# Optimization experiments

Hardware: AMD Instinct MI355X
Metric: run time of the kernel (lower is better)

## Reference

```python
import jax, jax.numpy as jnp
import numpy as np

B, N, CIN = 8, 16384, 256
G, K, C, H, L = 16, 128, 256, 8, 2


def setup_inputs() -> dict:
    key = jax.random.key(0)
    ks = jax.random.split(key, 8)
    f = lambda k, s: jax.random.normal(k, s, dtype=jnp.float32)
    return dict(
        x=f(ks[0], (B, N, CIN)),
        W_lin=f(ks[1], (CIN, C)) * 0.02,
        b_lin=jnp.zeros((C,), jnp.float32),
        emb=f(ks[2], (G, K, C)),  # learned_embedding ~ randn in torch
        in_proj_w=f(ks[3], (L, 3 * C, C)) * 0.02,
        in_proj_b=jnp.zeros((L, 3 * C), jnp.float32),
        out_w=f(ks[4], (L, C, C)) * 0.02,
        out_b=jnp.zeros((L, C), jnp.float32),
        lin_w=f(ks[5], (L, C, C)) * 0.02,
        lin_b=jnp.zeros((L, C), jnp.float32),
        ln1_w=jnp.ones((L, C), jnp.float32),
        ln1_b=jnp.zeros((L, C), jnp.float32),
        ln2_w=jnp.ones((L, C), jnp.float32),
        ln2_b=jnp.zeros((L, C), jnp.float32),
    )


def _layernorm(x, w, b, eps=1e-5):
    m = x.mean(-1, keepdims=True)
    v = jnp.var(x, axis=-1, keepdims=True)
    return (x - m) / jnp.sqrt(v + eps) * w + b


def reference(x, W_lin, b_lin, emb, in_proj_w, in_proj_b, out_w, out_b,
              lin_w, lin_b, ln1_w, ln1_b, ln2_w, ln2_b):
    B_, N_, Cin = x.shape
    T = N_ // G  # tokens per group
    # grouped projection: [B,G,T,C]
    x4 = x.reshape(B_, G, T, Cin) @ W_lin + b_lin
    # cross-attn scores [B,G,K,T]; softmax over the LATENT axis k (dim=-2)
    scores = jnp.einsum('gkd,bgtd->bgkt', emb, x4) * (1.0 / jnp.sqrt(jnp.float32(C)))
    attn = jax.nn.softmax(scores, axis=2)
    y = jnp.einsum('bgkt,bgtd->bgkd', attn, x4)  # [B,G,K,C]
    # torch MHA with batch_first=False: (B*G) is SEQUENCE, K is BATCH
    y = y.reshape(B_ * G, K, C)  # (S, Nb, C)
    S = B_ * G
    Dh = C // H
    scale = 1.0 / jnp.sqrt(jnp.float32(Dh))
    for i in range(L):
        qkv = y @ in_proj_w[i].T + in_proj_b[i]
        q, k, v = jnp.split(qkv, 3, axis=-1)
        q = q.reshape(S, K, H, Dh)
        k = k.reshape(S, K, H, Dh)
        v = v.reshape(S, K, H, Dh)
        s2 = jnp.einsum('snhd,tnhd->nhst', q, k) * scale  # (Nb,H,S,S)
        a = jax.nn.softmax(s2, axis=-1)
        o = jnp.einsum('nhst,tnhd->snhd', a, v).reshape(S, K, C)
        o = o @ out_w[i].T + out_b[i]
        y = _layernorm(o + y, ln1_w[i], ln1_b[i])
        y = _layernorm(y @ lin_w[i].T + lin_b[i] + y, ln2_w[i], ln2_b[i])
    out = y.reshape(B_, G * K, C)
    return (out, attn)
```

## Files before the change

kernel.cpp:

```cpp
#include <hip/hip_runtime.h>

typedef __attribute__((ext_vector_type(4))) float  f32x4;
typedef __attribute__((ext_vector_type(8))) short  s16x8;
typedef __attribute__((ext_vector_type(4))) short  s16x4;

static __device__ __forceinline__ short f2bf(float f) {
    unsigned int x = __builtin_bit_cast(unsigned int, f);
    x += 0x7fffu + ((x >> 16) & 1u);
    return (short)(x >> 16);
}

__global__ __launch_bounds__(256) void castall(
    const float* __restrict__ emb, const float* __restrict__ ipw,
    const float* __restrict__ outw, const float* __restrict__ linw,
    short* __restrict__ de, short* __restrict__ di,
    short* __restrict__ dg, short* __restrict__ dl)
{
    int q = blockIdx.x * 256 + threadIdx.x;
    const float* s; short* d; int o;
    if (q < 131072)      { s = emb;  d = de; o = q; }
    else if (q < 229376) { s = ipw;  d = di; o = q - 131072; }
    else if (q < 262144) { s = outw; d = dg; o = q - 229376; }
    else                 { s = linw; d = dl; o = q - 262144; }
    f32x4 v = *(const f32x4*)(s + (size_t)o * 4);
    s16x4 r;
    #pragma unroll
    for (int j = 0; j < 4; ++j) r[j] = f2bf(v[j]);
    *(s16x4*)(d + (size_t)o * 4) = r;
}

__global__ __launch_bounds__(256) void tcast256(const float* __restrict__ in,
                                                short* __restrict__ out) {
    out[blockIdx.x * 256 + threadIdx.x] = f2bf(in[threadIdx.x * 256 + blockIdx.x]);
}

template<bool AF32, bool OF32, bool OB16>
__global__ __launch_bounds__(256) void gemm_rb(
    const void* __restrict__ Av, const short* __restrict__ Bm,
    const float* __restrict__ bias,
    float* __restrict__ Cf, short* __restrict__ Cb,
    int M, int N)
{
    __shared__ short lsB[128 * 256];
    const int tid = threadIdx.x;
    const int m0 = blockIdx.x * 128;
    const int n0 = blockIdx.y * 128;
    const int lane = tid & 63;
    const int w = tid >> 6;
    const int wmi = w >> 1, wni = w & 1;
    const int lr = lane & 15, ko = lane >> 4;

    {
        const int r0 = tid >> 1, hb = tid & 1;
        const short* Bp = Bm + (size_t)(n0 + r0) * 256 + hb * 128;
        const int sw = (r0 & 7) << 4;
        char* dst = (char*)(lsB + r0 * 256);
        #pragma unroll
        for (int i = 0; i < 16; ++i) {
            int cb = (hb * 16 + i) * 16;
            *(s16x8*)(dst + (cb ^ sw)) = *(const s16x8*)(Bp + i * 8);
        }
    }
    __syncthreads();

    const int swr = (lr & 7) << 4;
    f32x4 acc[4][4] = {};
    #pragma unroll
    for (int ks = 0; ks < 8; ++ks) {
        const int k0 = ks * 32;
        s16x8 af[4];
        #pragma unroll
        for (int mt = 0; mt < 4; ++mt) {
            const int rowA = m0 + wmi * 64 + mt * 16 + lr;
            if constexpr (AF32) {
                const float* Ap = (const float*)Av + (size_t)rowA * 256 + k0 + ko * 8;
                f32x4 x0 = *(const f32x4*)Ap;
                f32x4 x1 = *(const f32x4*)(Ap + 4);
                #pragma unroll
                for (int j = 0; j < 4; ++j) { af[mt][j] = f2bf(x0[j]); af[mt][4 + j] = f2bf(x1[j]); }
            } else {
                const short* Ap = (const short*)Av + (size_t)rowA * 256 + k0 + ko * 8;
                af[mt] = *(const s16x8*)Ap;
            }
        }
        s16x8 bf[4];
        #pragma unroll
        for (int nt = 0; nt < 4; ++nt) {
            const int nrow = wni * 64 + nt * 16 + lr;
            bf[nt] = *(const s16x8*)((const char*)(lsB + nrow * 256) + ((k0 * 2 + ko * 16) ^ swr));
        }
        #pragma unroll
        for (int mt = 0; mt < 4; ++mt)
            #pragma unroll
            for (int nt = 0; nt < 4; ++nt)
                acc[mt][nt] = __builtin_amdgcn_mfma_f32_16x16x32_bf16(af[mt], bf[nt], acc[mt][nt], 0, 0, 0);
    }
    const int cr = ko * 4, cc = lr;
    #pragma unroll
    for (int mt = 0; mt < 4; ++mt)
    #pragma unroll
    for (int nt = 0; nt < 4; ++nt) {
        const int col = n0 + wni * 64 + nt * 16 + cc;
        const float bv = bias ? bias[col] : 0.f;
        #pragma unroll
        for (int j = 0; j < 4; ++j) {
            const int row = m0 + wmi * 64 + mt * 16 + cr + j;
            float v = acc[mt][nt][j] + bv;
            size_t idx = (size_t)row * N + col;
            if constexpr (OF32) Cf[idx] = v;
            if constexpr (OB16) Cb[idx] = f2bf(v);
        }
    }
}

__global__ __launch_bounds__(256) void scores_softmax(
    const short* __restrict__ embb, const short* __restrict__ x4b,
    float* __restrict__ attnF, short* __restrict__ attnB)
{
    __shared__ short lsA[128 * 256];
    float* redm = (float*)lsA;
    float* reds = redm + 256;
    const int tid = threadIdx.x;
    const int z = blockIdx.y;
    const int g = z & 15;
    const int t0 = blockIdx.x * 128;
    const short* A = embb + (size_t)g * 32768;
    const short* B = x4b + (size_t)z * 262144 + (size_t)t0 * 256;
    const int lane = tid & 63;
    const int w = tid >> 6;
    const int wmi = w >> 1, wni = w & 1;
    const int lr = lane & 15, ko = lane >> 4;

    {
        const int r0 = tid >> 1, hb = tid & 1;
        const short* Ap = A + (size_t)r0 * 256 + hb * 128;
        const int sw = (r0 & 7) << 4;
        char* dst = (char*)(lsA + r0 * 256);
        #pragma unroll
        for (int i = 0; i < 16; ++i) {
            int cb = (hb * 16 + i) * 16;
            *(s16x8*)(dst + (cb ^ sw)) = *(const s16x8*)(Ap + i * 8);
        }
    }
    __syncthreads();

    const int swr = (lr & 7) << 4;
    f32x4 acc[4][4] = {};
    #pragma unroll
    for (int ks = 0; ks < 8; ++ks) {
        const int k0 = ks * 32;
        s16x8 af[4];
        #pragma unroll
        for (int mt = 0; mt < 4; ++mt) {
            const int krow = wmi * 64 + mt * 16 + lr;
            af[mt] = *(const s16x8*)((const char*)(lsA + krow * 256) + ((k0 * 2 + ko * 16) ^ swr));
        }
        s16x8 bf[4];
        #pragma unroll
        for (int nt = 0; nt < 4; ++nt) {
            const int trow = wni * 64 + nt * 16 + lr;
            bf[nt] = *(const s16x8*)(B + (size_t)trow * 256 + k0 + ko * 8);
        }
        #pragma unroll
        for (int mt = 0; mt < 4; ++mt)
            #pragma unroll
            for (int nt = 0; nt < 4; ++nt)
                acc[mt][nt] = __builtin_amdgcn_mfma_f32_16x16x32_bf16(af[mt], bf[nt], acc[mt][nt], 0, 0, 0);
    }
    __syncthreads();

    const float scale = 0.0625f;
    float cm[4];
    #pragma unroll
    for (int nt = 0; nt < 4; ++nt) {
        float m = -1e30f;
        #pragma unroll
        for (int mt = 0; mt < 4; ++mt)
            #pragma unroll
            for (int j = 0; j < 4; ++j) m = fmaxf(m, acc[mt][nt][j]);
        m = fmaxf(m, __shfl_xor(m, 16));
        m = fmaxf(m, __shfl_xor(m, 32));
        cm[nt] = m * scale;
    }
    if (lane < 16) {
        #pragma unroll
        for (int nt = 0; nt < 4; ++nt)
            redm[wmi * 128 + wni * 64 + nt * 16 + lr] = cm[nt];
    }
    __syncthreads();
    float cmax[4];
    #pragma unroll
    for (int nt = 0; nt < 4; ++nt) {
        int c = wni * 64 + nt * 16 + lr;
        cmax[nt] = fmaxf(redm[c], redm[128 + c]);
    }
    float cs[4];
    #pragma unroll
    for (int nt = 0; nt < 4; ++nt) {
        float s = 0.f;
        #pragma unroll
        for (int mt = 0; mt < 4; ++mt)
            #pragma unroll
            for (int j = 0; j < 4; ++j) {
                float p = __expf(acc[mt][nt][j] * scale - cmax[nt]);
                acc[mt][nt][j] = p;
                s += p;
            }
        s += __shfl_xor(s, 16);
        s += __shfl_xor(s, 32);
        cs[nt] = s;
    }
    if (lane < 16) {
        #pragma unroll
        for (int nt = 0; nt < 4; ++nt)
            reds[wmi * 128 + wni * 64 + nt * 16 + lr] = cs[nt];
    }
    __syncthreads();
    #pragma unroll
    for (int nt = 0; nt < 4; ++nt) {
        int c = wni * 64 + nt * 16 + lr;
        float inv = 1.f / (reds[c] + reds[128 + c]);
        int col = t0 + c;
        #pragma unroll
        for (int mt = 0; mt < 4; ++mt)
            #pragma unroll
            for (int j = 0; j < 4; ++j) {
                int row = wmi * 64 + mt * 16 + ko * 4 + j;
                float a = acc[mt][nt][j] * inv;
                size_t idx = ((size_t)(z * 128 + row)) * 1024 + col;
                attnF[idx] = a;
                attnB[idx] = f2bf(a);
            }
    }
}

__global__ __launch_bounds__(256) void y_gemm(
    const short* __restrict__ attnB, const short* __restrict__ x4b,
    float* __restrict__ yF, short* __restrict__ yB)
{
    __shared__ short lsA[128 * 40];
    __shared__ short lsB[128 * 40];
    const int tid = threadIdx.x;
    const int z = blockIdx.y;
    const int d0 = blockIdx.x * 128;
    const short* A = attnB + (size_t)z * 131072;
    const short* X = x4b + (size_t)z * 262144 + d0;
    const int lane = tid & 63;
    const int w = tid >> 6;
    const int wmi = w >> 1, wni = w & 1;
    const int lr = lane & 15, ko = lane >> 4;
    const int r0 = tid >> 1, oc0 = (tid * 2) & 3;
    const int rb = tid >> 3, ocb = (tid * 2) & 15;

    const short* Ap = A + (size_t)r0 * 1024 + oc0 * 8;
    const short* Xp = X + (size_t)rb * 256 + ocb * 8;

    s16x8 pa0 = *(const s16x8*)(Ap);
    s16x8 pa1 = *(const s16x8*)(Ap + 8);
    s16x8 pv0 = *(const s16x8*)(Xp);
    s16x8 pv1 = *(const s16x8*)(Xp + 8);

    f32x4 acc[4][4] = {};
    for (int k0 = 0; k0 < 1024; k0 += 32) {
        *(s16x8*)&lsA[r0 * 40 + oc0 * 8]     = pa0;
        *(s16x8*)&lsA[r0 * 40 + oc0 * 8 + 8] = pa1;
        #pragma unroll
        for (int j = 0; j < 8; ++j) {
            int dd = ocb * 8 + j;
            lsB[dd * 40 + ((((rb >> 3) ^ ((dd >> 4) & 3)) << 3) | (rb & 7))] = pv0[j];
            int dd2 = dd + 8;
            lsB[dd2 * 40 + ((((rb >> 3) ^ ((dd2 >> 4) & 3)) << 3) | (rb & 7))] = pv1[j];
        }
        __syncthreads();
        if (k0 + 32 < 1024) {
            pa0 = *(const s16x8*)(Ap + k0 + 32);
            pa1 = *(const s16x8*)(Ap + k0 + 40);
            pv0 = *(const s16x8*)(Xp + (size_t)(k0 + 32) * 256);
            pv1 = *(const s16x8*)(Xp + (size_t)(k0 + 32) * 256 + 8);
        }
        #pragma unroll
        for (int mt = 0; mt < 4; ++mt) {
            s16x8 a = *(const s16x8*)&lsA[(wmi * 64 + mt * 16 + lr) * 40 + ko * 8];
            #pragma unroll
            for (int nt = 0; nt < 4; ++nt) {
                int dd = wni * 64 + nt * 16 + lr;
                s16x8 b = *(const s16x8*)&lsB[dd * 40 + ((ko ^ ((dd >> 4) & 3)) << 3)];
                acc[mt][nt] = __builtin_amdgcn_mfma_f32_16x16x32_bf16(a, b, acc[mt][nt], 0, 0, 0);
            }
        }
        __syncthreads();
    }
    const int cr = ko * 4, cc = lr;
    #pragma unroll
    for (int mt = 0; mt < 4; ++mt)
    #pragma unroll
    for (int nt = 0; nt < 4; ++nt)
        #pragma unroll
        for (int j = 0; j < 4; ++j) {
            int krow = wmi * 64 + mt * 16 + cr + j;
            int col = d0 + wni * 64 + nt * 16 + cc;
            float v = acc[mt][nt][j];
            size_t idx = ((size_t)(z * 128 + krow)) * 256 + col;
            yF[idx] = v;
            yB[idx] = f2bf(v);
        }
}

__global__ __launch_bounds__(256) void mha(
    const short* __restrict__ qkvb, short* __restrict__ ob)
{
    __shared__ short la[128 * 136];
    __shared__ short lvt[32 * 136];
    __shared__ float redm[2 * 128];
    __shared__ float reds[2 * 128];
    short* lq = la;
    short* lk = la + 128 * 40;
    const int tid = threadIdx.x;
    const int nb = blockIdx.x >> 3;
    const int h = blockIdx.x & 7;
    const int lane = tid & 63;
    const int w = tid >> 6;
    const int wmi = w >> 1, wni = w & 1;
    const int lr = lane & 15, ko = lane >> 4;
    const int sv = tid >> 1, oc0 = (tid * 2) & 3;
    {
        const short* qp = qkvb + ((size_t)sv * 128 + nb) * 768 + h * 32 + oc0 * 8;
        *(s16x8*)&lq[sv * 40 + oc0 * 8]     = *(const s16x8*)qp;
        *(s16x8*)&lq[sv * 40 + oc0 * 8 + 8] = *(const s16x8*)(qp + 8);
        const short* kp = qp + 256;
        *(s16x8*)&lk[sv * 40 + oc0 * 8]     = *(const s16x8*)kp;
        *(s16x8*)&lk[sv * 40 + oc0 * 8 + 8] = *(const s16x8*)(kp + 8);
        const short* vp = qp + 512;
        s16x8 v0 = *(const s16x8*)vp;
        s16x8 v1 = *(const s16x8*)(vp + 8);
        #pragma unroll
        for (int j = 0; j < 8; ++j) {
            lvt[(oc0 * 8 + j) * 136 + sv]     = v0[j];
            lvt[(oc0 * 8 + 8 + j) * 136 + sv] = v1[j];
        }
    }
    __syncthreads();
    f32x4 acc[4][4] = {};
    #pragma unroll
    for (int mt = 0; mt < 4; ++mt) {
        s16x8 a = *(const s16x8*)&lq[(wmi * 64 + mt * 16 + lr) * 40 + ko * 8];
        #pragma unroll
        for (int nt = 0; nt < 4; ++nt) {
            s16x8 b = *(const s16x8*)&lk[(wni * 64 + nt * 16 + lr) * 40 + ko * 8];
            acc[mt][nt] = __builtin_amdgcn_mfma_f32_16x16x32_bf16(a, b, acc[mt][nt], 0, 0, 0);
        }
    }
    const float scale = 0.1767766953f;
    float rm[4][4];
    #pragma unroll
    for (int mt = 0; mt < 4; ++mt)
        #pragma unroll
        for (int j = 0; j < 4; ++j) {
            float m = -1e30f;
            #pragma unroll
            for (int nt = 0; nt < 4; ++nt) m = fmaxf(m, acc[mt][nt][j]);
            m = fmaxf(m, __shfl_xor(m, 1));
            m = fmaxf(m, __shfl_xor(m, 2));
            m = fmaxf(m, __shfl_xor(m, 4));
            m = fmaxf(m, __shfl_xor(m, 8));
            rm[mt][j] = m * scale;
        }
    if (lr == 0) {
        #pragma unroll
        for (int mt = 0; mt < 4; ++mt)
            #pragma unroll
            for (int j = 0; j < 4; ++j)
                redm[wni * 128 + wmi * 64 + mt * 16 + ko * 4 + j] = rm[mt][j];
    }
    __syncthreads();
    float rs[4][4];
    #pragma unroll
    for (int mt = 0; mt < 4; ++mt)
        #pragma unroll
        for (int j = 0; j < 4; ++j) {
            int row = wmi * 64 + mt * 16 + ko * 4 + j;
            float mx = fmaxf(redm[row], redm[128 + row]);
            float s = 0.f;
            #pragma unroll
            for (int nt = 0; nt < 4; ++nt) {
                float p = __expf(acc[mt][nt][j] * scale - mx);
                acc[mt][nt][j] = p;
                s += p;
            }
            s += __shfl_xor(s, 1);
            s += __shfl_xor(s, 2);
            s += __shfl_xor(s, 4);
            s += __shfl_xor(s, 8);
            rs[mt][j] = s;
        }
    if (lr == 0) {
        #pragma unroll
        for (int mt = 0; mt < 4; ++mt)
            #pragma unroll
            for (int j = 0; j < 4; ++j)
                reds[wni * 128 + wmi * 64 + mt * 16 + ko * 4 + j] = rs[mt][j];
    }
    __syncthreads();
    #pragma unroll
    for (int mt = 0; mt < 4; ++mt)
        #pragma unroll
        for (int j = 0; j < 4; ++j) {
            int row = wmi * 64 + mt * 16 + ko * 4 + j;
            float inv = 1.f / (reds[row] + reds[128 + row]);
            #pragma unroll
            for (int nt = 0; nt < 4; ++nt) {
                int col = wni * 64 + nt * 16 + lr;
                la[row * 136 + col] = f2bf(acc[mt][nt][j] * inv);
            }
        }
    __syncthreads();
    f32x4 acc2[2][2] = {};
    #pragma unroll
    for (int ks = 0; ks < 4; ++ks)
        #pragma unroll
        for (int mt = 0; mt < 2; ++mt) {
            s16x8 a = *(const s16x8*)&la[(w * 32 + mt * 16 + lr) * 136 + ks * 32 + ko * 8];
            #pragma unroll
            for (int nt = 0; nt < 2; ++nt) {
                s16x8 b = *(const s16x8*)&lvt[(nt * 16 + lr) * 136 + ks * 32 + ko * 8];
                acc2[mt][nt] = __builtin_amdgcn_mfma_f32_16x16x32_bf16(a, b, acc2[mt][nt], 0, 0, 0);
            }
        }
    const int cr = ko * 4, cc = lr;
    #pragma unroll
    for (int mt = 0; mt < 2; ++mt)
    #pragma unroll
    for (int nt = 0; nt < 2; ++nt)
        #pragma unroll
        for (int j = 0; j < 4; ++j) {
            int s = w * 32 + mt * 16 + cr + j;
            int d = nt * 16 + cc;
            ob[((size_t)s * 128 + nb) * 256 + h * 32 + d] = f2bf(acc2[mt][nt][j]);
        }
}

__global__ __launch_bounds__(256) void ln_res(
    const float* __restrict__ zin, const float* __restrict__ res,
    const float* __restrict__ gw, const float* __restrict__ gb,
    float* __restrict__ outF, short* __restrict__ outB)
{
    const int row = blockIdx.x * 4 + (threadIdx.x >> 6);
    const int lane = threadIdx.x & 63;
    const size_t base = (size_t)row * 256 + lane * 4;
    f32x4 a = *(const f32x4*)(zin + base);
    f32x4 b = *(const f32x4*)(res + base);
    f32x4 v;
    #pragma unroll
    for (int j = 0; j < 4; ++j) v[j] = a[j] + b[j];
    float s1 = v[0] + v[1] + v[2] + v[3];
    float s2 = v[0]*v[0] + v[1]*v[1] + v[2]*v[2] + v[3]*v[3];
    #pragma unroll
    for (int o = 1; o < 64; o <<= 1) {
        s1 += __shfl_xor(s1, o);
        s2 += __shfl_xor(s2, o);
    }
    float m = s1 * 0.00390625f;
    float var = s2 * 0.00390625f - m * m;
    float rstd = rsqrtf(var + 1e-5f);
    f32x4 g = *(const f32x4*)(gw + lane * 4);
    f32x4 bb = *(const f32x4*)(gb + lane * 4);
    f32x4 o; s16x4 obv;
    #pragma unroll
    for (int j = 0; j < 4; ++j) {
        o[j] = (v[j] - m) * rstd * g[j] + bb[j];
        obv[j] = f2bf(o[j]);
    }
    *(f32x4*)(outF + base) = o;
    *(s16x4*)(outB + base) = obv;
}

extern "C" void kernel_launch(void* const* d_in, const int* in_sizes, int n_in,
                              void* d_out, int out_size, void* d_ws, size_t ws_size,
                              hipStream_t stream)
{
    const float* x    = (const float*)d_in[0];
    const float* Wlin = (const float*)d_in[1];
    const float* blin = (const float*)d_in[2];
    const float* emb  = (const float*)d_in[3];
    const float* ipw  = (const float*)d_in[4];
    const float* ipb  = (const float*)d_in[5];
    const float* outw = (const float*)d_in[6];
    const float* outb = (const float*)d_in[7];
    const float* linw = (const float*)d_in[8];
    const float* linb = (const float*)d_in[9];
    const float* ln1w = (const float*)d_in[10];
    const float* ln1b = (const float*)d_in[11];
    const float* ln2w = (const float*)d_in[12];
    const float* ln2b = (const float*)d_in[13];

    char* ws = (char*)d_ws;
    short* x4_b   = (short*)(ws);
    short* attn_b = (short*)(ws + 67108864);
    float* yF     = (float*)(ws + 100663296);
    short* y_b    = (short*)(ws + 117440512);
    char*  wb     = ws + 125829120;
    short* WT_b   = (short*)(wb);
    short* emb_b  = (short*)(wb + 131072);
    short* inw_b  = (short*)(wb + 131072 + 1048576);
    short* outw_b = (short*)(wb + 131072 + 1048576 + 786432);
    short* linw_b = (short*)(wb + 131072 + 1048576 + 786432 + 262144);
    short* qkv_b  = (short*)(ws);
    short* o_b    = (short*)(ws + 25165824);
    float* op     = (float*)(ws + 33554432);

    float* out_y    = (float*)d_out;
    float* out_attn = (float*)d_out + 4194304;

    castall<<<dim3(1152), dim3(256), 0, stream>>>(emb, ipw, outw, linw,
                                                  emb_b, inw_b, outw_b, linw_b);
    tcast256<<<dim3(256), dim3(256), 0, stream>>>(Wlin, WT_b);

    gemm_rb<true, false, true><<<dim3(1024, 2), dim3(256), 0, stream>>>(
        x, WT_b, blin, nullptr, x4_b, 131072, 256);
    scores_softmax<<<dim3(8, 128), dim3(256), 0, stream>>>(emb_b, x4_b, out_attn, attn_b);
    y_gemm<<<dim3(2, 128), dim3(256), 0, stream>>>(attn_b, x4_b, yF, y_b);

    for (int i = 0; i < 2; ++i) {
        gemm_rb<false, false, true><<<dim3(128, 6), dim3(256), 0, stream>>>(
            y_b, inw_b + i * 196608, ipb + i * 768, nullptr, qkv_b, 16384, 768);
        mha<<<dim3(1024), dim3(256), 0, stream>>>(qkv_b, o_b);
        gemm_rb<false, true, false><<<dim3(128, 2), dim3(256), 0, stream>>>(
            o_b, outw_b + i * 65536, outb + i * 256, op, nullptr, 16384, 256);
        ln_res<<<dim3(4096), dim3(256), 0, stream>>>(
            op, yF, ln1w + i * 256, ln1b + i * 256, yF, y_b);
        gemm_rb<false, true, false><<<dim3(128, 2), dim3(256), 0, stream>>>(
            y_b, linw_b + i * 65536, linb + i * 256, op, nullptr, 16384, 256);
        ln_res<<<dim3(4096), dim3(256), 0, stream>>>(
            op, yF, ln2w + i * 256, ln2b + i * 256, (i == 1) ? out_y : yF, y_b);
    }
}
```

Before: 586.4 us.

## Double-buffer LDS tiles with register prefetch across GEMM kernels, shrink N tiles

Replaces the GEMMs that staged all of B (128x256) in LDS and read A straight from global memory with a K-step double-buffered scheme. Both A and B tiles of 32 columns are staged through LDS and the next tile is prefetched into registers while MFMAs run on the current one. This applies to the generic GEMM, the scores+softmax kernel and y_gemm. The N tile is halved for the smaller GEMMs and y_gemm to double the block count for better occupancy. The cost is more syncthreads per K step and smaller per-block reuse of A.

```diff
diff --git a/kernel.cpp b/kernel.cpp
--- a/kernel.cpp
+++ b/kernel.cpp
@@ -34,73 +34,110 @@
     out[blockIdx.x * 256 + threadIdx.x] = f2bf(in[threadIdx.x * 256 + blockIdx.x]);
 }
 
-template<bool AF32, bool OF32, bool OB16>
-__global__ __launch_bounds__(256) void gemm_rb(
+template<bool AF32, int NT, bool OF32, bool OB16>
+__global__ __launch_bounds__(256) void gemm2p(
     const void* __restrict__ Av, const short* __restrict__ Bm,
     const float* __restrict__ bias,
     float* __restrict__ Cf, short* __restrict__ Cb,
-    int M, int N)
-{
-    __shared__ short lsB[128 * 256];
+    int M, int N, int K)
+{
+    constexpr int BN = NT * 32;
+    __shared__ short lsA[2][128][40];
+    __shared__ short lsB[2][BN][40];
     const int tid = threadIdx.x;
     const int m0 = blockIdx.x * 128;
-    const int n0 = blockIdx.y * 128;
-    const int lane = tid & 63;
-    const int w = tid >> 6;
+    const int n0 = blockIdx.y * BN;
+    const int lane = tid & 63, w = tid >> 6;
     const int wmi = w >> 1, wni = w & 1;
     const int lr = lane & 15, ko = lane >> 4;
-
-    {
-        const int r0 = tid >> 1, hb = tid & 1;
-        const short* Bp = Bm + (size_t)(n0 + r0) * 256 + hb * 128;
-        const int sw = (r0 & 7) << 4;
-        char* dst = (char*)(lsB + r0 * 256);
-        #pragma unroll
-        for (int i = 0; i < 16; ++i) {
-            int cb = (hb * 16 + i) * 16;
-            *(s16x8*)(dst + (cb ^ sw)) = *(const s16x8*)(Bp + i * 8);
-        }
-    }
-    __syncthreads();
-
-    const int swr = (lr & 7) << 4;
-    f32x4 acc[4][4] = {};
-    #pragma unroll
-    for (int ks = 0; ks < 8; ++ks) {
-        const int k0 = ks * 32;
-        s16x8 af[4];
-        #pragma unroll
-        for (int mt = 0; mt < 4; ++mt) {
-            const int rowA = m0 + wmi * 64 + mt * 16 + lr;
-            if constexpr (AF32) {
-                const float* Ap = (const float*)Av + (size_t)rowA * 256 + k0 + ko * 8;
-                f32x4 x0 = *(const f32x4*)Ap;
-                f32x4 x1 = *(const f32x4*)(Ap + 4);
-                #pragma unroll
-                for (int j = 0; j < 4; ++j) { af[mt][j] = f2bf(x0[j]); af[mt][4 + j] = f2bf(x1[j]); }
-            } else {
-                const short* Ap = (const short*)Av + (size_t)rowA * 256 + k0 + ko * 8;
-                af[mt] = *(const s16x8*)Ap;
-            }
-        }
-        s16x8 bf[4];
-        #pragma unroll
-        for (int nt = 0; nt < 4; ++nt) {
-            const int nrow = wni * 64 + nt * 16 + lr;
-            bf[nt] = *(const s16x8*)((const char*)(lsB + nrow * 256) + ((k0 * 2 + ko * 16) ^ swr));
-        }
-        #pragma unroll
-        for (int mt = 0; mt < 4; ++mt)
-            #pragma unroll
-            for (int nt = 0; nt < 4; ++nt)
-                acc[mt][nt] = __builtin_amdgcn_mfma_f32_16x16x32_bf16(af[mt], bf[nt], acc[mt][nt], 0, 0, 0);
-    }
+    const int nK = K >> 5;
+    const float* Af = (const float*)Av;
+    const short* Ah = (const short*)Av;
+
+    f32x4 pf0[4], pf1[4];
+    s16x8 pa0[2], pa1[2];
+    s16x8 pb0[2], pb1[2];
+
+#define LDA(PF, PA, T) do { const int k0_ = (T) * 32;                               \
+    if constexpr (AF32) {                                                           \
+        _Pragma("unroll")                                                           \
+        for (int i = 0; i < 4; ++i) { int c = i * 256 + tid;                        \
+            PF[i] = *(const f32x4*)(Af + (size_t)(m0 + (c >> 3)) * K + k0_ + (c & 7) * 4); } \
+    } else {                                                                        \
+        _Pragma("unroll")                                                           \
+        for (int i = 0; i < 2; ++i) { int c = i * 256 + tid;                        \
+            PA[i] = *(const s16x8*)(Ah + (size_t)(m0 + (c >> 2)) * K + k0_ + (c & 3) * 8); } \
+    } } while (0)
+
+#define LDB(PB, T) do { const int k0_ = (T) * 32;                                   \
+    if constexpr (NT == 4) {                                                        \
+        _Pragma("unroll")                                                           \
+        for (int i = 0; i < 2; ++i) { int c = i * 256 + tid;                        \
+            PB[i] = *(const s16x8*)(Bm + (size_t)(n0 + (c >> 2)) * K + k0_ + (c & 3) * 8); } \
+    } else {                                                                        \
+        PB[0] = *(const s16x8*)(Bm + (size_t)(n0 + (tid >> 2)) * K + k0_ + (tid & 3) * 8); \
+    } } while (0)
+
+#define WR(BUF, PF, PA, PB) do {                                                    \
+    if constexpr (AF32) {                                                           \
+        _Pragma("unroll")                                                           \
+        for (int i = 0; i < 4; ++i) { int c = i * 256 + tid; s16x4 r_;              \
+            _Pragma("unroll")                                                       \
+            for (int j = 0; j < 4; ++j) r_[j] = f2bf(PF[i][j]);                     \
+            *(s16x4*)&lsA[BUF][c >> 3][(c & 7) * 4] = r_; }                         \
+    } else {                                                                        \
+        _Pragma("unroll")                                                           \
+        for (int i = 0; i < 2; ++i) { int c = i * 256 + tid;                        \
+            *(s16x8*)&lsA[BUF][c >> 2][(c & 3) * 8] = PA[i]; }                      \
+    }                                                                               \
+    if constexpr (NT == 4) {                                                        \
+        _Pragma("unroll")                                                           \
+        for (int i = 0; i < 2; ++i) { int c = i * 256 + tid;                        \
+            *(s16x8*)&lsB[BUF][c >> 2][(c & 3) * 8] = PB[i]; }                      \
+    } else {                                                                        \
+        *(s16x8*)&lsB[BUF][tid >> 2][(tid & 3) * 8] = PB[0];                        \
+    } } while (0)
+
+#define MFMA(BUF) do {                                                              \
+    s16x8 afr[4], bfr[NT];                                                          \
+    _Pragma("unroll")                                                               \
+    for (int mt = 0; mt < 4; ++mt)                                                  \
+        afr[mt] = *(const s16x8*)&lsA[BUF][wmi * 64 + mt * 16 + lr][ko * 8];        \
+    _Pragma("unroll")                                                               \
+    for (int nt = 0; nt < NT; ++nt)                                                 \
+        bfr[nt] = *(const s16x8*)&lsB[BUF][wni * (NT * 16) + nt * 16 + lr][ko * 8]; \
+    _Pragma("unroll")                                                               \
+    for (int mt = 0; mt < 4; ++mt)                                                  \
+        _Pragma("unroll")                                                           \
+        for (int nt = 0; nt < NT; ++nt)                                             \
+            acc[mt][nt] = __builtin_amdgcn_mfma_f32_16x16x32_bf16(afr[mt], bfr[nt], acc[mt][nt], 0, 0, 0); \
+    } while (0)
+
+    f32x4 acc[4][NT] = {};
+    LDA(pf0, pa0, 0); LDB(pb0, 0);
+    WR(0, pf0, pa0, pb0);
+    LDA(pf0, pa0, 1); LDB(pb0, 1);
+    __syncthreads();
+    for (int t = 0; t < nK; t += 2) {
+        if (t + 2 < nK) { LDA(pf1, pa1, t + 2); LDB(pb1, t + 2); }
+        MFMA(0);
+        WR(1, pf0, pa0, pb0);
+        __syncthreads();
+        if (t + 3 < nK) { LDA(pf0, pa0, t + 3); LDB(pb0, t + 3); }
+        MFMA(1);
+        if (t + 2 < nK) WR(0, pf1, pa1, pb1);
+        __syncthreads();
+    }
+#undef LDA
+#undef LDB
+#undef WR
+#undef MFMA
     const int cr = ko * 4, cc = lr;
     #pragma unroll
     for (int mt = 0; mt < 4; ++mt)
     #pragma unroll
-    for (int nt = 0; nt < 4; ++nt) {
-        const int col = n0 + wni * 64 + nt * 16 + cc;
+    for (int nt = 0; nt < NT; ++nt) {
+        const int col = n0 + wni * (NT * 16) + nt * 16 + cc;
         const float bv = bias ? bias[col] : 0.f;
         #pragma unroll
         for (int j = 0; j < 4; ++j) {
@@ -117,57 +154,67 @@
     const short* __restrict__ embb, const short* __restrict__ x4b,
     float* __restrict__ attnF, short* __restrict__ attnB)
 {
-    __shared__ short lsA[128 * 256];
-    float* redm = (float*)lsA;
-    float* reds = redm + 256;
+    __shared__ short lsA[2][128][40];
+    __shared__ short lsB[2][128][40];
+    __shared__ float redm[256];
+    __shared__ float reds[256];
     const int tid = threadIdx.x;
     const int z = blockIdx.y;
     const int g = z & 15;
     const int t0 = blockIdx.x * 128;
     const short* A = embb + (size_t)g * 32768;
     const short* B = x4b + (size_t)z * 262144 + (size_t)t0 * 256;
-    const int lane = tid & 63;
-    const int w = tid >> 6;
+    const int lane = tid & 63, w = tid >> 6;
     const int wmi = w >> 1, wni = w & 1;
     const int lr = lane & 15, ko = lane >> 4;
 
-    {
-        const int r0 = tid >> 1, hb = tid & 1;
-        const short* Ap = A + (size_t)r0 * 256 + hb * 128;
-        const int sw = (r0 & 7) << 4;
-        char* dst = (char*)(lsA + r0 * 256);
-        #pragma unroll
-        for (int i = 0; i < 16; ++i) {
-            int cb = (hb * 16 + i) * 16;
-            *(s16x8*)(dst + (cb ^ sw)) = *(const s16x8*)(Ap + i * 8);
-        }
-    }
-    __syncthreads();
-
-    const int swr = (lr & 7) << 4;
+    s16x8 pa0[2], pa1[2], pb0[2], pb1[2];
+
+#define SLD(PA, PB, T) do { const int k0_ = (T) * 32;                               \
+    _Pragma("unroll")                                                               \
+    for (int i = 0; i < 2; ++i) { int c = i * 256 + tid;                            \
+        PA[i] = *(const s16x8*)(A + (size_t)(c >> 2) * 256 + k0_ + (c & 3) * 8);    \
+        PB[i] = *(const s16x8*)(B + (size_t)(c >> 2) * 256 + k0_ + (c & 3) * 8); }  \
+    } while (0)
+#define SWR(BUF, PA, PB) do {                                                       \
+    _Pragma("unroll")                                                               \
+    for (int i = 0; i < 2; ++i) { int c = i * 256 + tid;                            \
+        *(s16x8*)&lsA[BUF][c >> 2][(c & 3) * 8] = PA[i];                            \
+        *(s16x8*)&lsB[BUF][c >> 2][(c & 3) * 8] = PB[i]; }                          \
+    } while (0)
+#define SMFMA(BUF) do {                                                             \
+    s16x8 afr[4], bfr[4];                                                           \
+    _Pragma("unroll")                                                               \
+    for (int mt = 0; mt < 4; ++mt)                                                  \
+        afr[mt] = *(const s16x8*)&lsA[BUF][wmi * 64 + mt * 16 + lr][ko * 8];        \
+    _Pragma("unroll")                                                               \
+    for (int nt = 0; nt < 4; ++nt)                                                  \
+        bfr[nt] = *(const s16x8*)&lsB[BUF][wni * 64 + nt * 16 + lr][ko * 8];        \
+    _Pragma("unroll")                                                               \
+    for (int mt = 0; mt < 4; ++mt)                                                  \
+        _Pragma("unroll")                                                           \
+        for (int nt = 0; nt < 4; ++nt)                                              \
+            acc[mt][nt] = __builtin_amdgcn_mfma_f32_16x16x32_bf16(afr[mt], bfr[nt], acc[mt][nt], 0, 0, 0); \
+    } while (0)
+
     f32x4 acc[4][4] = {};
-    #pragma unroll
-    for (int ks = 0; ks < 8; ++ks) {
-        const int k0 = ks * 32;
-        s16x8 af[4];
-        #pragma unroll
-        for (int mt = 0; mt < 4; ++mt) {
-            const int krow = wmi * 64 + mt * 16 + lr;
-            af[mt] = *(const s16x8*)((const char*)(lsA + krow * 256) + ((k0 * 2 + ko * 16) ^ swr));
-        }
-        s16x8 bf[4];
-        #pragma unroll
-        for (int nt = 0; nt < 4; ++nt) {
-            const int trow = wni * 64 + nt * 16 + lr;
-            bf[nt] = *(const s16x8*)(B + (size_t)trow * 256 + k0 + ko * 8);
-        }
-        #pragma unroll
-        for (int mt = 0; mt < 4; ++mt)
-            #pragma unroll
-            for (int nt = 0; nt < 4; ++nt)
-                acc[mt][nt] = __builtin_amdgcn_mfma_f32_16x16x32_bf16(af[mt], bf[nt], acc[mt][nt], 0, 0, 0);
-    }
-    __syncthreads();
+    SLD(pa0, pb0, 0);
+    SWR(0, pa0, pb0);
+    SLD(pa0, pb0, 1);
+    __syncthreads();
+    for (int t = 0; t < 8; t += 2) {
+        if (t + 2 < 8) SLD(pa1, pb1, t + 2);
+        SMFMA(0);
+        SWR(1, pa0, pb0);
+        __syncthreads();
+        if (t + 3 < 8) SLD(pa0, pb0, t + 3);
+        SMFMA(1);
+        if (t + 2 < 8) SWR(0, pa1, pb1);
+        __syncthreads();
+    }
+#undef SLD
+#undef SWR
+#undef SMFMA
 
     const float scale = 0.0625f;
     float cm[4];
@@ -238,67 +285,76 @@
     const short* __restrict__ attnB, const short* __restrict__ x4b,
     float* __restrict__ yF, short* __restrict__ yB)
 {
-    __shared__ short lsA[128 * 40];
-    __shared__ short lsB[128 * 40];
+    __shared__ short lsA[2][128][40];
+    __shared__ short lsB[2][64][40];
     const int tid = threadIdx.x;
     const int z = blockIdx.y;
-    const int d0 = blockIdx.x * 128;
+    const int d0 = blockIdx.x * 64;
     const short* A = attnB + (size_t)z * 131072;
     const short* X = x4b + (size_t)z * 262144 + d0;
-    const int lane = tid & 63;
-    const int w = tid >> 6;
+    const int lane = tid & 63, w = tid >> 6;
     const int wmi = w >> 1, wni = w & 1;
     const int lr = lane & 15, ko = lane >> 4;
-    const int r0 = tid >> 1, oc0 = (tid * 2) & 3;
-    const int rb = tid >> 3, ocb = (tid * 2) & 15;
-
-    const short* Ap = A + (size_t)r0 * 1024 + oc0 * 8;
-    const short* Xp = X + (size_t)rb * 256 + ocb * 8;
-
-    s16x8 pa0 = *(const s16x8*)(Ap);
-    s16x8 pa1 = *(const s16x8*)(Ap + 8);
-    s16x8 pv0 = *(const s16x8*)(Xp);
-    s16x8 pv1 = *(const s16x8*)(Xp + 8);
-
-    f32x4 acc[4][4] = {};
-    for (int k0 = 0; k0 < 1024; k0 += 32) {
-        *(s16x8*)&lsA[r0 * 40 + oc0 * 8]     = pa0;
-        *(s16x8*)&lsA[r0 * 40 + oc0 * 8 + 8] = pa1;
-        #pragma unroll
-        for (int j = 0; j < 8; ++j) {
-            int dd = ocb * 8 + j;
-            lsB[dd * 40 + ((((rb >> 3) ^ ((dd >> 4) & 3)) << 3) | (rb & 7))] = pv0[j];
-            int dd2 = dd + 8;
-            lsB[dd2 * 40 + ((((rb >> 3) ^ ((dd2 >> 4) & 3)) << 3) | (rb & 7))] = pv1[j];
-        }
+    const int kr = tid >> 3, dc = tid & 7;
+    const int slot = kr ^ ((tid & 3) << 3);
+
+    s16x8 pa0[2], pa1[2], pb0, pb1;
+
+#define YLD(PA, PB, T) do { const int k0_ = (T) * 32;                               \
+    _Pragma("unroll")                                                               \
+    for (int i = 0; i < 2; ++i) { int c = i * 256 + tid;                            \
+        PA[i] = *(const s16x8*)(A + (size_t)(c >> 2) * 1024 + k0_ + (c & 3) * 8); } \
+    PB = *(const s16x8*)(X + (size_t)(k0_ + kr) * 256 + dc * 8);                    \
+    } while (0)
+#define YWR(BUF, PA, PB) do {                                                       \
+    _Pragma("unroll")                                                               \
+    for (int i = 0; i < 2; ++i) { int c = i * 256 + tid;                            \
+        *(s16x8*)&lsA[BUF][c >> 2][(c & 3) * 8] = PA[i]; }                          \
+    _Pragma("unroll")                                                               \
+    for (int j = 0; j < 8; ++j) lsB[BUF][dc * 8 + j][slot] = PB[j];                 \
+    } while (0)
+#define YMFMA(BUF) do {                                                             \
+    s16x8 afr[4], bfr[2];                                                           \
+    _Pragma("unroll")                                                               \
+    for (int mt = 0; mt < 4; ++mt)                                                  \
+        afr[mt] = *(const s16x8*)&lsA[BUF][wmi * 64 + mt * 16 + lr][ko * 8];        \
+    _Pragma("unroll")                                                               \
+    for (int nt = 0; nt < 2; ++nt) { int dd = wni * 32 + nt * 16 + lr;              \
+        bfr[nt] = *(const s16x8*)&lsB[BUF][dd][(ko * 8) ^ (((dd >> 3) & 3) << 3)]; }\
+    _Pragma("unroll")                                                               \
+    for (int mt = 0; mt < 4; ++mt)                                                  \
+        _Pragma("unroll")                                                           \
+        for (int nt = 0; nt < 2; ++nt)                                              \
+            acc[mt][nt] = __builtin_amdgcn_mfma_f32_16x16x32_bf16(afr[mt], bfr[nt], acc[mt][nt], 0, 0, 0); \
+    } while (0)
+
+    f32x4 acc[4][2] = {};
+    YLD(pa0, pb0, 0);
+    YWR(0, pa0, pb0);
+    YLD(pa0, pb0, 1);
+    __syncthreads();
+    for (int t = 0; t < 32; t += 2) {
+        if (t + 2 < 32) YLD(pa1, pb1, t + 2);
+        YMFMA(0);
+        YWR(1, pa0, pb0);
         __syncthreads();
-        if (k0 + 32 < 1024) {
-            pa0 = *(const s16x8*)(Ap + k0 + 32);
-            pa1 = *(const s16x8*)(Ap + k0 + 40);
-            pv0 = *(const s16x8*)(Xp + (size_t)(k0 + 32) * 256);
-            pv1 = *(const s16x8*)(Xp + (size_t)(k0 + 32) * 256 + 8);
-        }
-        #pragma unroll
-        for (int mt = 0; mt < 4; ++mt) {
-            s16x8 a = *(const s16x8*)&lsA[(wmi * 64 + mt * 16 + lr) * 40 + ko * 8];
-            #pragma unroll
-            for (int nt = 0; nt < 4; ++nt) {
-                int dd = wni * 64 + nt * 16 + lr;
-                s16x8 b = *(const s16x8*)&lsB[dd * 40 + ((ko ^ ((dd >> 4) & 3)) << 3)];
-                acc[mt][nt] = __builtin_amdgcn_mfma_f32_16x16x32_bf16(a, b, acc[mt][nt], 0, 0, 0);
-            }
-        }
+        if (t + 3 < 32) YLD(pa0, pb0, t + 3);
+        YMFMA(1);
+        if (t + 2 < 32) YWR(0, pa1, pb1);
         __syncthreads();
     }
+#undef YLD
+#undef YWR
+#undef YMFMA
     const int cr = ko * 4, cc = lr;
     #pragma unroll
     for (int mt = 0; mt < 4; ++mt)
     #pragma unroll
-    for (int nt = 0; nt < 4; ++nt)
+    for (int nt = 0; nt < 2; ++nt)
         #pragma unroll
         for (int j = 0; j < 4; ++j) {
             int krow = wmi * 64 + mt * 16 + cr + j;
-            int col = d0 + wni * 64 + nt * 16 + cc;
+            int col = d0 + wni * 32 + nt * 16 + cc;
             float v = acc[mt][nt][j];
             size_t idx = ((size_t)(z * 128 + krow)) * 256 + col;
             yF[idx] = v;
@@ -515,21 +571,21 @@
                                                   emb_b, inw_b, outw_b, linw_b);
     tcast256<<<dim3(256), dim3(256), 0, stream>>>(Wlin, WT_b);
 
-    gemm_rb<true, false, true><<<dim3(1024, 2), dim3(256), 0, stream>>>(
-        x, WT_b, blin, nullptr, x4_b, 131072, 256);
+    gemm2p<true, 4, false, true><<<dim3(1024, 2), dim3(256), 0, stream>>>(
+        x, WT_b, blin, nullptr, x4_b, 131072, 256, 256);
     scores_softmax<<<dim3(8, 128), dim3(256), 0, stream>>>(emb_b, x4_b, out_attn, attn_b);
-    y_gemm<<<dim3(2, 128), dim3(256), 0, stream>>>(attn_b, x4_b, yF, y_b);
+    y_gemm<<<dim3(4, 128), dim3(256), 0, stream>>>(attn_b, x4_b, yF, y_b);
 
     for (int i = 0; i < 2; ++i) {
-        gemm_rb<false, false, true><<<dim3(128, 6), dim3(256), 0, stream>>>(
-            y_b, inw_b + i * 196608, ipb + i * 768, nullptr, qkv_b, 16384, 768);
+        gemm2p<false, 2, false, true><<<dim3(128, 12), dim3(256), 0, stream>>>(
+            y_b, inw_b + i * 196608, ipb + i * 768, nullptr, qkv_b, 16384, 768, 256);
         mha<<<dim3(1024), dim3(256), 0, stream>>>(qkv_b, o_b);
-        gemm_rb<false, true, false><<<dim3(128, 2), dim3(256), 0, stream>>>(
-            o_b, outw_b + i * 65536, outb + i * 256, op, nullptr, 16384, 256);
+        gemm2p<false, 2, true, false><<<dim3(128, 4), dim3(256), 0, stream>>>(
+            o_b, outw_b + i * 65536, outb + i * 256, op, nullptr, 16384, 256, 256);
         ln_res<<<dim3(4096), dim3(256), 0, stream>>>(
             op, yF, ln1w + i * 256, ln1b + i * 256, yF, y_b);
-        gemm_rb<false, true, false><<<dim3(128, 2), dim3(256), 0, stream>>>(
-            y_b, linw_b + i * 65536, linb + i * 256, op, nullptr, 16384, 256);
+        gemm2p<false, 2, true, false><<<dim3(128, 4), dim3(256), 0, stream>>>(
+            y_b, linw_b + i * 65536, linb + i * 256, op, nullptr, 16384, 256, 256);
         ln_res<<<dim3(4096), dim3(256), 0, stream>>>(
             op, yF, ln2w + i * 256, ln2b + i * 256, (i == 1) ? out_y : yF, y_b);
     }
```

Measured after the change: 521.9 us. 11.0% less time.
